# Optimization experiments

Hardware: AMD Instinct MI355X
Metric: run time of the kernel (lower is better)

## Reference

```python
import jax, jax.numpy as jnp
import numpy as np

GROUPS = 32
EPS = 1e-3  # keras GroupNormalization default epsilon


def setup_inputs() -> dict:
    key = jax.random.key(0)
    ks = jax.random.split(key, 7)
    B, H, W, C = 16, 32, 32, 512
    inputs = jax.random.normal(ks[0], (B, H, W, C), dtype=jnp.float32)
    gamma = jnp.ones((C,), dtype=jnp.float32)
    beta = jnp.zeros((C,), dtype=jnp.float32)
    # EinsumDense 'bhwc,cae->bhwae', output last dims (C,3), bias axes 'ae'
    W_qkv = jax.random.normal(ks[1], (C, C, 3), dtype=jnp.float32) / np.sqrt(C)
    b_qkv = jnp.zeros((C, 3), dtype=jnp.float32)
    # EinsumDense 'bhwc,cd->bhwd', bias axes 'd'
    W_out = jax.random.normal(ks[2], (C, C), dtype=jnp.float32) / np.sqrt(C)
    b_out = jnp.zeros((C,), dtype=jnp.float32)
    return {
        "inputs": inputs,
        "gamma": gamma,
        "beta": beta,
        "W_qkv": W_qkv,
        "b_qkv": b_qkv,
        "W_out": W_out,
        "b_out": b_out,
    }


def group_norm(x, gamma, beta):
    B, H, W, C = x.shape
    g = GROUPS
    xr = x.reshape(B, H, W, g, C // g)
    mean = jnp.mean(xr, axis=(1, 2, 4), keepdims=True)
    var = jnp.var(xr, axis=(1, 2, 4), keepdims=True)
    xn = (xr - mean) * jax.lax.rsqrt(var + EPS)
    return xn.reshape(B, H, W, C) * gamma + beta


def reference(inputs, gamma, beta, W_qkv, b_qkv, W_out, b_out):
    B, H, W, C = inputs.shape
    scale = C ** (-0.5)
    x = group_norm(inputs, gamma, beta)
    # QKV projection: bhwc,cae->bhwae  (+ bias over 'ae')
    qkv = jnp.einsum("bhwc,cae->bhwae", x, W_qkv) + b_qkv
    q, k, v = qkv[..., 0], qkv[..., 1], qkv[..., 2]  # each [B,H,W,C]
    # full spatial attention: [B,H,W,H,W]
    attn = jnp.einsum("bhwc,btlc->bhwtl", q, k) * scale
    attn = attn.reshape(B, H, W, H * W)
    attn = jax.nn.softmax(attn, axis=-1)
    attn = attn.reshape(B, H, W, H, W)
    out = jnp.einsum("bhwtl,btlc->bhwc", attn, v)
    out = jnp.einsum("bhwc,cd->bhwd", out, W_out) + b_out
    return inputs + out
```

## Files before the change

kernel.cpp:

```cpp
#include <hip/hip_runtime.h>
#include <hip/hip_bf16.h>

#define NB    16
#define SP    1024
#define NC    512
#define NG    32
#define MTOT  (NB*SP)
#define EPSV  1e-3f
#define SCALE 0.04419417382415922f

using f32x4   = __attribute__((ext_vector_type(4))) float;
using short8  = __attribute__((ext_vector_type(8))) short;
using short4v = __attribute__((ext_vector_type(4))) short;
using bf16x8v = __attribute__((ext_vector_type(8))) __bf16;

__device__ __forceinline__ unsigned short f2bf(float f) {
  union { float f; unsigned int u; } x; x.f = f;
  unsigned int u = x.u;
  unsigned int r = (u + 0x7FFFu + ((u >> 16) & 1u)) >> 16;
  return (unsigned short)r;
}

#define GLOAD_LDS16(g, l)                                                     \
  __builtin_amdgcn_global_load_lds(                                           \
      (const __attribute__((address_space(1))) void*)(g),                     \
      (__attribute__((address_space(3))) void*)(l), 16, 0, 0)

__global__ __launch_bounds__(256) void gn_stats_k(const float* __restrict__ x,
                                                  float2* __restrict__ stats) {
  int bg = blockIdx.x;
  int b = bg >> 5, g = bg & 31;
  int tid = threadIdx.x;
  int c = tid & 15, s0 = tid >> 4;
  const float* base = x + (long)b * SP * NC + g * 16 + c;
  float s = 0.f, ss = 0.f;
  for (int sp = s0; sp < SP; sp += 16) {
    float v = base[(long)sp * NC];
    s += v; ss += v * v;
  }
  for (int o = 32; o > 0; o >>= 1) { s += __shfl_xor(s, o); ss += __shfl_xor(ss, o); }
  __shared__ float rs[4], rss[4];
  int lane = tid & 63, wv = tid >> 6;
  if (lane == 0) { rs[wv] = s; rss[wv] = ss; }
  __syncthreads();
  if (tid == 0) {
    float S = rs[0] + rs[1] + rs[2] + rs[3];
    float SS = rss[0] + rss[1] + rss[2] + rss[3];
    float mean = S * (1.f / 16384.f);
    float var  = SS * (1.f / 16384.f) - mean * mean;
    stats[bg] = make_float2(mean, rsqrtf(var + EPSV));
  }
}

__global__ __launch_bounds__(256) void gn_apply_k(const float* __restrict__ x,
                                                  const float2* __restrict__ stats,
                                                  const float* __restrict__ gamma,
                                                  const float* __restrict__ beta,
                                                  unsigned short* __restrict__ xn) {
  long t = (long)blockIdx.x * 256 + threadIdx.x;
  long base = t * 8;
  int c = (int)(base & 511);
  int b = (int)(base >> 19);
  float2 st = stats[b * NG + (c >> 4)];
  f32x4 v0 = *reinterpret_cast<const f32x4*>(x + base);
  f32x4 v1 = *reinterpret_cast<const f32x4*>(x + base + 4);
  f32x4 g0 = *reinterpret_cast<const f32x4*>(gamma + c);
  f32x4 g1 = *reinterpret_cast<const f32x4*>(gamma + c + 4);
  f32x4 b0 = *reinterpret_cast<const f32x4*>(beta + c);
  f32x4 b1 = *reinterpret_cast<const f32x4*>(beta + c + 4);
  short8 o;
  #pragma unroll
  for (int q = 0; q < 4; ++q) {
    float sc = st.y * g0[q];
    o[q] = (short)f2bf(v0[q] * sc + (b0[q] - st.x * sc));
  }
  #pragma unroll
  for (int q = 0; q < 4; ++q) {
    float sc = st.y * g1[q];
    o[q + 4] = (short)f2bf(v1[q] * sc + (b1[q] - st.x * sc));
  }
  *reinterpret_cast<short8*>(xn + base) = o;
}

__global__ __launch_bounds__(256) void pack_wqkv_k(const float* __restrict__ W,
                                                   const float* __restrict__ bq,
                                                   unsigned short* __restrict__ Wp,
                                                   float* __restrict__ bp) {
  int idx = blockIdx.x * 256 + threadIdx.x;
  int n = idx >> 9, c = idx & 511;
  int e = n >> 9, a = n & 511;
  Wp[idx] = f2bf(W[((long)c * 512 + a) * 3 + e]);
  if (idx < 1536) {
    int e2 = idx >> 9, a2 = idx & 511;
    bp[idx] = bq[a2 * 3 + e2];
  }
}

__global__ __launch_bounds__(256) void pack_wout_k(const float* __restrict__ W,
                                                   unsigned short* __restrict__ Wp) {
  int idx = blockIdx.x * 256 + threadIdx.x;
  int n = idx >> 9, c = idx & 511;
  Wp[idx] = f2bf(W[(long)c * 512 + n]);
}

__global__ void transpose_v_k(const unsigned short* __restrict__ qkv,
                              unsigned short* __restrict__ vT) {
  __shared__ unsigned short t[32][33];
  int bs = blockIdx.x, bc = blockIdx.y, b = blockIdx.z;
  int tx = threadIdx.x, ty = threadIdx.y;
  #pragma unroll
  for (int k = 0; k < 4; ++k) {
    int s = bs * 32 + ty + k * 8, c = bc * 32 + tx;
    t[ty + k * 8][tx] = qkv[((long)b * SP + s) * 1536 + 1024 + c];
  }
  __syncthreads();
  #pragma unroll
  for (int k = 0; k < 4; ++k) {
    int c = bc * 32 + ty + k * 8, s = bs * 32 + tx;
    vT[((long)b * NC + c) * SP + s] = t[tx][ty + k * 8];
  }
}

__global__ __launch_bounds__(256) void softmax_k(float* __restrict__ S) {
  long row = blockIdx.x;
  const float* r = S + row * 1024;
  int tid = threadIdx.x, lane = tid & 63, wv = tid >> 6;
  f32x4 v = *reinterpret_cast<const f32x4*>(r + tid * 4);
  float m = fmaxf(fmaxf(v[0], v[1]), fmaxf(v[2], v[3]));
  for (int o = 32; o > 0; o >>= 1) m = fmaxf(m, __shfl_xor(m, o));
  __shared__ float wm[4], ws[4];
  if (lane == 0) wm[wv] = m;
  __syncthreads();
  float rmax = fmaxf(fmaxf(wm[0], wm[1]), fmaxf(wm[2], wm[3]));
  float e[4]; float ssum = 0.f;
  #pragma unroll
  for (int q = 0; q < 4; ++q) { e[q] = __expf(v[q] - rmax); ssum += e[q]; }
  for (int o = 32; o > 0; o >>= 1) ssum += __shfl_xor(ssum, o);
  if (lane == 0) ws[wv] = ssum;
  __syncthreads();
  float inv = 1.f / (ws[0] + ws[1] + ws[2] + ws[3]);
  short4v pv;
  #pragma unroll
  for (int q = 0; q < 4; ++q) pv[q] = (short)f2bf(e[q] * inv);
  unsigned short* P = reinterpret_cast<unsigned short*>(S);
  *reinterpret_cast<short4v*>(&P[row * 2048 + tid * 4]) = pv;
}

template <int EPI>
__global__ __launch_bounds__(256) void gemm_tn(
    const unsigned short* __restrict__ Ap, long strideA, int lda,
    const unsigned short* __restrict__ Bp, long strideB, int ldb,
    void* __restrict__ Op, long strideO, int ldo,
    const float* __restrict__ bias, const float* __restrict__ residual,
    int K, float scale) {
  __shared__ unsigned short As[128 * 32];
  __shared__ unsigned short Bs[128 * 32];
  const int tid = threadIdx.x;
  const int lane = tid & 63, wv = tid >> 6;
  const int bm = blockIdx.y * 128, bn = blockIdx.x * 128;
  const int z = blockIdx.z;
  const unsigned short* Ag = Ap + (long)z * strideA;
  const unsigned short* Bg = Bp + (long)z * strideB;

  const int srow = lane >> 2;
  const int scol = (lane & 3) * 8;
  const int wm = (wv >> 1) * 64, wn = (wv & 1) * 64;
  const int lrow = lane & 15, lk = (lane >> 4) * 8;

  f32x4 acc[4][4] = {};
  for (int kt = 0; kt < K; kt += 32) {
    #pragma unroll
    for (int it = 0; it < 2; ++it) {
      int chunk = it * 4 + wv;
      int row = chunk * 16 + srow;
      GLOAD_LDS16(Ag + (long)(bm + row) * lda + kt + scol, As + chunk * 512);
      GLOAD_LDS16(Bg + (long)(bn + row) * ldb + kt + scol, Bs + chunk * 512);
    }
    __syncthreads();

    short8 afr[4], bfr[4];
    #pragma unroll
    for (int i = 0; i < 4; ++i)
      afr[i] = *reinterpret_cast<const short8*>(&As[(wm + i * 16 + lrow) * 32 + lk]);
    #pragma unroll
    for (int j = 0; j < 4; ++j)
      bfr[j] = *reinterpret_cast<const short8*>(&Bs[(wn + j * 16 + lrow) * 32 + lk]);
    #pragma unroll
    for (int i = 0; i < 4; ++i)
      #pragma unroll
      for (int j = 0; j < 4; ++j)
        acc[i][j] = __builtin_amdgcn_mfma_f32_16x16x32_bf16(
            __builtin_bit_cast(bf16x8v, afr[i]),
            __builtin_bit_cast(bf16x8v, bfr[j]), acc[i][j], 0, 0, 0);
    __syncthreads();
  }

  const int colb = bn + wn + (lane & 15);
  #pragma unroll
  for (int i = 0; i < 4; ++i) {
    #pragma unroll
    for (int r = 0; r < 4; ++r) {
      int rowg = bm + wm + i * 16 + (lane >> 4) * 4 + r;
      #pragma unroll
      for (int j = 0; j < 4; ++j) {
        int colg = colb + j * 16;
        float v = acc[i][j][r];
        if (EPI == 0) {
          v += bias[colg];
          ((unsigned short*)Op)[(long)z * strideO + (long)rowg * ldo + colg] = f2bf(v);
        } else if (EPI == 1) {
          ((float*)Op)[(long)z * strideO + (long)rowg * ldo + colg] = v * scale;
        } else if (EPI == 2) {
          ((unsigned short*)Op)[(long)z * strideO + (long)rowg * ldo + colg] = f2bf(v);
        } else {
          v += bias[colg] + residual[(long)rowg * ldo + colg];
          ((float*)Op)[(long)rowg * ldo + colg] = v;
        }
      }
    }
  }
}

extern "C" void kernel_launch(void* const* d_in, const int* in_sizes, int n_in,
                              void* d_out, int out_size, void* d_ws, size_t ws_size,
                              hipStream_t stream) {
  const float* x     = (const float*)d_in[0];
  const float* gamma = (const float*)d_in[1];
  const float* beta  = (const float*)d_in[2];
  const float* Wqkv  = (const float*)d_in[3];
  const float* bqkv  = (const float*)d_in[4];
  const float* Wout  = (const float*)d_in[5];
  const float* bout  = (const float*)d_in[6];
  float* out = (float*)d_out;

  char* ws = (char*)d_ws;
  float2*         stats = (float2*)(ws + 0);
  unsigned short* wqkvP = (unsigned short*)(ws + 4096);
  float*          bqP   = (float*)(ws + 1576960);
  unsigned short* woutT = (unsigned short*)(ws + 1583104);
  unsigned short* qkv   = (unsigned short*)(ws + 2107392);
  unsigned short* vT    = (unsigned short*)(ws + 52439040);
  float*          Sbuf  = (float*)(ws + 69216256);
  unsigned short* attn  = (unsigned short*)(ws + 136325120);
  unsigned short* xn    = (unsigned short*)(ws + 153102336);

  gn_stats_k<<<512, 256, 0, stream>>>(x, stats);
  gn_apply_k<<<4096, 256, 0, stream>>>(x, stats, gamma, beta, xn);
  pack_wqkv_k<<<3072, 256, 0, stream>>>(Wqkv, bqkv, wqkvP, bqP);
  pack_wout_k<<<1024, 256, 0, stream>>>(Wout, woutT);

  gemm_tn<0><<<dim3(12, 128, 1), 256, 0, stream>>>(
      xn, 0L, NC, wqkvP, 0L, NC, qkv, 0L, 1536,
      bqP, nullptr, NC, 1.f);

  transpose_v_k<<<dim3(32, 16, 16), dim3(32, 8), 0, stream>>>(qkv, vT);

  gemm_tn<1><<<dim3(8, 8, 16), 256, 0, stream>>>(
      qkv, (long)SP * 1536, 1536, qkv + 512, (long)SP * 1536, 1536,
      Sbuf, (long)SP * SP, SP, nullptr, nullptr, NC, SCALE);

  softmax_k<<<MTOT, 256, 0, stream>>>(Sbuf);

  gemm_tn<2><<<dim3(4, 8, 16), 256, 0, stream>>>(
      (const unsigned short*)Sbuf, (long)SP * 2048, 2048, vT, (long)NC * SP, SP,
      attn, (long)SP * NC, NC, nullptr, nullptr, SP, 1.f);

  gemm_tn<3><<<dim3(4, 128, 1), 256, 0, stream>>>(
      attn, 0L, NC, woutT, 0L, NC, out, 0L, NC,
      bout, x, NC, 1.f);
}
```

Baseline: 299.7 us.

## Store attention scores in bf16 and remap GEMM workgroups across XCDs

The QK^T GEMM now writes its scaled scores as bf16 instead of fp32. Softmax reads bf16 and writes the probabilities in place with a dense stride, which halves score traffic through the S buffer. Separately, every GEMM remaps its flat workgroup index in groups of eight so that neighbouring tiles land on the same XCD, aiming at better L2 reuse. The cost is precision: logits are rounded to bf16 before softmax, and the remap assumes the tile count divides evenly by eight.

```diff
diff --git a/kernel.cpp b/kernel.cpp
--- a/kernel.cpp
+++ b/kernel.cpp
@@ -19,6 +19,10 @@
   unsigned int u = x.u;
   unsigned int r = (u + 0x7FFFu + ((u >> 16) & 1u)) >> 16;
   return (unsigned short)r;
+}
+__device__ __forceinline__ float bf2f(unsigned short b) {
+  union { unsigned int u; float f; } x; x.u = ((unsigned int)b) << 16;
+  return x.f;
 }
 
 #define GLOAD_LDS16(g, l)                                                     \
@@ -121,11 +125,14 @@
   }
 }
 
-__global__ __launch_bounds__(256) void softmax_k(float* __restrict__ S) {
+__global__ __launch_bounds__(256) void softmax_k(unsigned short* __restrict__ S) {
   long row = blockIdx.x;
-  const float* r = S + row * 1024;
+  unsigned short* r = S + row * 1024;
   int tid = threadIdx.x, lane = tid & 63, wv = tid >> 6;
-  f32x4 v = *reinterpret_cast<const f32x4*>(r + tid * 4);
+  short4v raw = *reinterpret_cast<const short4v*>(r + tid * 4);
+  float v[4];
+  #pragma unroll
+  for (int q = 0; q < 4; ++q) v[q] = bf2f((unsigned short)raw[q]);
   float m = fmaxf(fmaxf(v[0], v[1]), fmaxf(v[2], v[3]));
   for (int o = 32; o > 0; o >>= 1) m = fmaxf(m, __shfl_xor(m, o));
   __shared__ float wm[4], ws[4];
@@ -142,8 +149,7 @@
   short4v pv;
   #pragma unroll
   for (int q = 0; q < 4; ++q) pv[q] = (short)f2bf(e[q] * inv);
-  unsigned short* P = reinterpret_cast<unsigned short*>(S);
-  *reinterpret_cast<short4v*>(&P[row * 2048 + tid * 4]) = pv;
+  *reinterpret_cast<short4v*>(r + tid * 4) = pv;
 }
 
 template <int EPI>
@@ -157,7 +163,12 @@
   __shared__ unsigned short Bs[128 * 32];
   const int tid = threadIdx.x;
   const int lane = tid & 63, wv = tid >> 6;
-  const int bm = blockIdx.y * 128, bn = blockIdx.x * 128;
+
+  const int nwg  = gridDim.x * gridDim.y;
+  const int flat = blockIdx.y * gridDim.x + blockIdx.x;
+  const int w    = (flat & 7) * (nwg >> 3) + (flat >> 3);
+  const int bn = (w % gridDim.x) * 128;
+  const int bm = (w / gridDim.x) * 128;
   const int z = blockIdx.z;
   const unsigned short* Ag = Ap + (long)z * strideA;
   const unsigned short* Bg = Bp + (long)z * strideB;
@@ -208,10 +219,8 @@
         if (EPI == 0) {
           v += bias[colg];
           ((unsigned short*)Op)[(long)z * strideO + (long)rowg * ldo + colg] = f2bf(v);
-        } else if (EPI == 1) {
-          ((float*)Op)[(long)z * strideO + (long)rowg * ldo + colg] = v * scale;
         } else if (EPI == 2) {
-          ((unsigned short*)Op)[(long)z * strideO + (long)rowg * ldo + colg] = f2bf(v);
+          ((unsigned short*)Op)[(long)z * strideO + (long)rowg * ldo + colg] = f2bf(v * scale);
         } else {
           v += bias[colg] + residual[(long)rowg * ldo + colg];
           ((float*)Op)[(long)rowg * ldo + colg] = v;
@@ -240,7 +249,7 @@
   unsigned short* woutT = (unsigned short*)(ws + 1583104);
   unsigned short* qkv   = (unsigned short*)(ws + 2107392);
   unsigned short* vT    = (unsigned short*)(ws + 52439040);
-  float*          Sbuf  = (float*)(ws + 69216256);
+  unsigned short* Sbuf  = (unsigned short*)(ws + 69216256);
   unsigned short* attn  = (unsigned short*)(ws + 136325120);
   unsigned short* xn    = (unsigned short*)(ws + 153102336);
 
@@ -255,14 +264,14 @@
 
   transpose_v_k<<<dim3(32, 16, 16), dim3(32, 8), 0, stream>>>(qkv, vT);
 
-  gemm_tn<1><<<dim3(8, 8, 16), 256, 0, stream>>>(
+  gemm_tn<2><<<dim3(8, 8, 16), 256, 0, stream>>>(
       qkv, (long)SP * 1536, 1536, qkv + 512, (long)SP * 1536, 1536,
       Sbuf, (long)SP * SP, SP, nullptr, nullptr, NC, SCALE);
 
   softmax_k<<<MTOT, 256, 0, stream>>>(Sbuf);
 
   gemm_tn<2><<<dim3(4, 8, 16), 256, 0, stream>>>(
-      (const unsigned short*)Sbuf, (long)SP * 2048, 2048, vT, (long)NC * SP, SP,
+      Sbuf, (long)SP * SP, SP, vT, (long)NC * SP, SP,
       attn, (long)SP * NC, NC, nullptr, nullptr, SP, 1.f);
 
   gemm_tn<3><<<dim3(4, 128, 1), 256, 0, stream>>>(
```

Result: faster. 291.8 us (-2.6%).
